# Performance work log

Hardware: AMD Instinct MI355X
Metric: run time of the kernel (lower is better)

Reference implementation:

```python
import jax, jax.numpy as jnp
import numpy as np

EPS = 1e-12  # torch F.normalize default eps


def conv1x1(x, w, b):
    # x: [N,C,H,W], w: [K,C], b: [K]
    return jnp.einsum('nchw,kc->nkhw', x, w) + b[None, :, None, None]


def forward_sa(f1, f2, cw1, cb1, cw2, cb2):
    n, _, h, w = f1.shape
    c1 = conv1x1(f1, cw1, cb1)  # [N,1,H,W]
    c2 = conv1x1(f2, cw2, cb2)
    c1 = jax.nn.softmax(c1.reshape(n, h * w), axis=1).reshape(n, 1, h, w)
    c2 = jax.nn.softmax(c2.reshape(n, h * w), axis=1).reshape(n, 1, h, w)
    return c1 * f1, c2 * f2


def l2norm_ch(x):
    # torch F.normalize(x) -> p=2 over dim=1 with eps clamp
    n = jnp.sqrt(jnp.sum(x * x, axis=1, keepdims=True))
    return x / jnp.maximum(n, EPS)


def forward_ca(f1, f2, pw1, pb1, pw2, pb2):
    N, C, H, W = f1.shape
    f1_cl = conv1x1(f1, pw1, pb1).reshape(N, -1, H * W)  # [N,Cl,HW]
    f2_cl = conv1x1(f2, pw2, pb2).reshape(N, -1, H * W)
    # A[n,p,q] = sum_c f2_cl[n,c,p] * f1_cl[n,c,q]  -> [N,HW,HW]
    A_c = jnp.tanh(jnp.einsum('ncp,ncq->npq', f2_cl, f1_cl))
    f1_v = f1.reshape(N, C, H * W)
    f2_v = f2.reshape(N, C, H * W)
    # f1_hat = f1_v @ A_c^T ; f2_hat = f2_v @ A_c
    f1_hat = jnp.einsum('ncp,nqp->ncq', f1_v, A_c).reshape(N, C, H, W)
    f2_hat = jnp.einsum('ncp,npq->ncq', f2_v, A_c).reshape(N, C, H, W)
    return l2norm_ch(f1_hat), l2norm_ch(f2_hat)


def setup_inputs() -> dict:
    key = jax.random.key(0)
    ks = jax.random.split(key, 10)
    N, C, H, W = 2, 256, 64, 64
    Cl = C // 16
    sc = 1.0 / np.sqrt(C)
    return {
        'f1': jax.random.normal(ks[0], (N, C, H, W), jnp.float32),
        'f2': jax.random.normal(ks[1], (N, C, H, W), jnp.float32),
        'pw1': jax.random.normal(ks[2], (Cl, C), jnp.float32) * sc,
        'pb1': jax.random.normal(ks[3], (Cl,), jnp.float32) * sc,
        'pw2': jax.random.normal(ks[4], (Cl, C), jnp.float32) * sc,
        'pb2': jax.random.normal(ks[5], (Cl,), jnp.float32) * sc,
        'cw1': jax.random.normal(ks[6], (1, C), jnp.float32) * sc,
        'cb1': jax.random.normal(ks[7], (1,), jnp.float32) * sc,
        'cw2': jax.random.normal(ks[8], (1, C), jnp.float32) * sc,
        'cb2': jax.random.normal(ks[9], (1,), jnp.float32) * sc,
    }


def reference(f1, f2, pw1, pb1, pw2, pb2, cw1, cb1, cw2, cb2):
    f1_1, f2_1 = forward_sa(f1, f2, cw1, cb1, cw2, cb2)
    f1_hat, f2_hat = forward_ca(f1_1, f2_1, pw1, pb1, pw2, pb2)
    fp1_hat = jax.nn.relu(f1_hat + f1)
    fp2_hat = jax.nn.relu(f2_hat + f2)
    f1_2, f2_2 = forward_sa(fp1_hat, fp2_hat, cw1, cb1, cw2, cb2)
    # Original calls forward_ca(f1_2, f2_2) again but discards the result
    # and returns (f1_2, f2_2); the dead call is omitted (identical output).
    return (f1_2, f2_2)
```

## Files before the change

### kernel.cpp

```cpp
#include <hip/hip_runtime.h>
#include <hip/hip_bf16.h>
#include <math.h>

#define N_B 2
#define C_CH 256
#define HW_SZ 4096
#define CL_CH 16

typedef __bf16 bf16x8 __attribute__((ext_vector_type(8)));
typedef float f32x4 __attribute__((ext_vector_type(4)));
typedef float f32x16 __attribute__((ext_vector_type(16)));

__device__ __forceinline__ unsigned short f2bf(float x){
  __hip_bfloat16 b = __float2bfloat16(x);
  return *reinterpret_cast<unsigned short*>(&b);
}
__device__ __forceinline__ unsigned int pack_bf2(float a, float b){
  return (unsigned int)f2bf(a) | ((unsigned int)f2bf(b) << 16);
}
__device__ __forceinline__ float tanh_fast(float x){
  float e = __expf(2.0f * x);
  return 1.0f - 2.0f / (1.0f + e);
}
__device__ __forceinline__ void gload16(const void* gsrc, void* lds_dst){
  __builtin_amdgcn_global_load_lds(
      (const __attribute__((address_space(1))) unsigned int*)gsrc,
      (__attribute__((address_space(3))) unsigned int*)lds_dst, 16, 0, 0);
}

__global__ void k_conv1(const float* __restrict__ f1, const float* __restrict__ f2,
                        const float* __restrict__ w1, const float* __restrict__ w2,
                        const float* __restrict__ b1, const float* __restrict__ b2,
                        float* __restrict__ cv){
  const int i = blockIdx.z, n = blockIdx.y, t = threadIdx.x;
  const int ql = t & 63, cg = t >> 6;
  const int q = blockIdx.x * 64 + ql;
  const float* f = (i ? f2 : f1) + n * C_CH * HW_SZ;
  const float* w = i ? w2 : w1;
  __shared__ float ws[C_CH];
  __shared__ float red[4][72];
  ws[t] = w[t];
  __syncthreads();
  float acc = 0.f;
  #pragma unroll 8
  for (int c = cg * 64; c < cg * 64 + 64; ++c)
    acc += f[c * HW_SZ + q] * ws[c];
  red[cg][ql] = acc;
  __syncthreads();
  if (t < 64){
    float s = red[0][t] + red[1][t] + red[2][t] + red[3][t] + (i ? b2[0] : b1[0]);
    cv[(i * 2 + n) * HW_SZ + blockIdx.x * 64 + t] = s;
  }
}

__global__ void k_softmax(const float* __restrict__ cv, float* __restrict__ pr){
  const int r = blockIdx.x, t = threadIdx.x;
  const float* x = cv + r * HW_SZ;
  float* y = pr + r * HW_SZ;
  __shared__ float red[256];
  float v[16];
  float m = -1e30f;
  #pragma unroll
  for (int j = 0; j < 16; j++){ v[j] = x[j * 256 + t]; m = fmaxf(m, v[j]); }
  red[t] = m; __syncthreads();
  for (int s = 128; s > 0; s >>= 1){ if (t < s) red[t] = fmaxf(red[t], red[t + s]); __syncthreads(); }
  m = red[0]; __syncthreads();
  float sum = 0.f;
  #pragma unroll
  for (int j = 0; j < 16; j++){ v[j] = __expf(v[j] - m); sum += v[j]; }
  red[t] = sum; __syncthreads();
  for (int s = 128; s > 0; s >>= 1){ if (t < s) red[t] += red[t + s]; __syncthreads(); }
  const float inv = 1.0f / red[0];
  #pragma unroll
  for (int j = 0; j < 16; j++) y[j * 256 + t] = v[j] * inv;
}

__global__ void k_scale_cl(const float* __restrict__ f1, const float* __restrict__ f2,
                           const float* __restrict__ pr,
                           const float* __restrict__ pw1, const float* __restrict__ pw2,
                           const float* __restrict__ pb1, const float* __restrict__ pb2,
                           unsigned short* __restrict__ fs1, unsigned short* __restrict__ fs2,
                           unsigned short* __restrict__ clT1, unsigned short* __restrict__ clT2){
  const int i = blockIdx.z, n = blockIdx.y, t = threadIdx.x;
  const int ql = t & 63, cg = t >> 6;
  const int q = blockIdx.x * 64 + ql;
  const float* f = (i ? f2 : f1) + n * C_CH * HW_SZ;
  unsigned short* fs = (i ? fs2 : fs1) + n * C_CH * HW_SZ;
  unsigned short* clT = (i ? clT2 : clT1) + n * 32 * HW_SZ;
  const float* pw = i ? pw2 : pw1;
  const float* pb = i ? pb2 : pb1;
  __shared__ float wls[CL_CH * C_CH];
  __shared__ float red[4][CL_CH][66];
  #pragma unroll
  for (int j = 0; j < 16; j++) wls[j * 256 + t] = pw[j * 256 + t];
  __syncthreads();
  const float p = pr[(i * 2 + n) * HW_SZ + q];
  float acc[16];
  #pragma unroll
  for (int k = 0; k < 16; k++) acc[k] = 0.f;
  for (int c = cg * 64; c < cg * 64 + 64; ++c){
    float vv = f[c * HW_SZ + q] * p;
    fs[c * HW_SZ + q] = f2bf(vv);
    #pragma unroll
    for (int k = 0; k < 16; k++) acc[k] += wls[k * 256 + c] * vv;
  }
  #pragma unroll
  for (int k = 0; k < 16; k++) red[cg][k][ql] = acc[k];
  __syncthreads();
  #pragma unroll
  for (int j = 0; j < 4; j++){
    int e = j * 256 + t; int k = e >> 6, qq = e & 63;
    float s = red[0][k][qq] + red[1][k][qq] + red[2][k][qq] + red[3][k][qq] + pb[k];
    clT[(blockIdx.x * 64 + qq) * 32 + k] = f2bf(s);
  }
  if (t < 128){
    uint4 zv = {0u, 0u, 0u, 0u};
    int qq = t >> 1, half = t & 1;
    *reinterpret_cast<uint4*>(&clT[(blockIdx.x * 64 + qq) * 32 + 16 + half * 8]) = zv;
  }
}

__global__ __launch_bounds__(512, 2) void k_hat(
    const unsigned short* __restrict__ fs1, const unsigned short* __restrict__ fs2,
    const unsigned short* __restrict__ clT1, const unsigned short* __restrict__ clT2,
    float* __restrict__ hat1, float* __restrict__ hat2,
    float* __restrict__ pt1, float* __restrict__ pt2){
  const int t = threadIdx.x;
  const int bid = blockIdx.x;
  const int xcd = bid & 7, slot = bid >> 3;
  const int z = xcd >> 1;
  const int n = z & 1, i = z >> 1;
  const int x = slot * 2 + (xcd & 1);
  const int qt = x >> 1, ph = x & 1;
  const int q0 = qt * 128;
  const int pbase = ph * 2048;

  const unsigned short* fs = (i ? fs2 : fs1) + n * C_CH * HW_SZ;
  const unsigned short* uT = (i ? clT1 : clT2) + n * 32 * HW_SZ;
  const unsigned short* vT = (i ? clT2 : clT1) + n * 32 * HW_SZ;
  float* out = (ph ? (i ? pt2 : pt1) : (i ? hat2 : hat1)) + n * C_CH * HW_SZ;

  __shared__ __align__(16) unsigned short fsA[2][C_CH * 64];
  __shared__ __align__(16) unsigned short vB[2][64 * 32];
  __shared__ __align__(16) unsigned short aT[128 * 64];

  const int wv = t >> 6, l = t & 63;
  const int g4 = l >> 4, lr16 = l & 15;
  const int g2 = l >> 5, lr32 = l & 31;

  const int pfw = wv & 3;
  const int qfb = (wv >> 2) * 4;
  const int cblk = wv & 3, qblk = wv >> 2;

  bf16x8 ub0 = *reinterpret_cast<const bf16x8*>(&uT[(q0 + (qfb + 0) * 16 + lr16) * 32 + g4 * 8]);
  bf16x8 ub1 = *reinterpret_cast<const bf16x8*>(&uT[(q0 + (qfb + 1) * 16 + lr16) * 32 + g4 * 8]);
  bf16x8 ub2 = *reinterpret_cast<const bf16x8*>(&uT[(q0 + (qfb + 2) * 16 + lr16) * 32 + g4 * 8]);
  bf16x8 ub3 = *reinterpret_cast<const bf16x8*>(&uT[(q0 + (qfb + 3) * 16 + lr16) * 32 + g4 * 8]);

  f32x16 acc00, acc01, acc10, acc11;
  #pragma unroll
  for (int r = 0; r < 16; ++r){ acc00[r] = 0.f; acc01[r] = 0.f; acc10[r] = 0.f; acc11[r] = 0.f; }
  const f32x4 zz = {0.f, 0.f, 0.f, 0.f};

  int fs_src[4];
  #pragma unroll
  for (int it = 0; it < 4; ++it){
    int d = it * 512 + t; int c = d >> 3, s = d & 7;
    int u = s ^ (c & 7) ^ (((c >> 3) & 1) << 2);
    fs_src[it] = c * (HW_SZ * 2) + u * 16;
  }
  int vt_src;
  {
    int j = t & 255; int p = j >> 2, s = j & 3;
    int u = s ^ (p & 3) ^ ((p >> 2) & 3);
    vt_src = p * 64 + u * 16;
  }
  int vbr;
  {
    int p = pfw * 16 + lr16;
    vbr = p * 64 + ((g4 ^ (p & 3) ^ ((p >> 2) & 3)) << 4);
  }
  unsigned atw0;
  {
    int qd = qfb * 16 + lr16;
    int sw = (pfw * 2 + (g4 >> 1)) ^ (qd & 7) ^ (((qd >> 3) & 1) << 2);
    atw0 = qd * 128 + sw * 16 + (g4 & 1) * 8;
  }
  unsigned afo[2], bqo[2];
  #pragma unroll
  for (int cfi = 0; cfi < 2; ++cfi){
    int crow = cblk * 64 + cfi * 32 + lr32;
    afo[cfi] = crow * 128 + ((g2 ^ (crow & 7) ^ (((crow >> 3) & 1) << 2)) << 4);
  }
  #pragma unroll
  for (int qq = 0; qq < 2; ++qq){
    int qrow = qblk * 64 + qq * 32 + lr32;
    bqo[qq] = qrow * 128 + ((g2 ^ (qrow & 7) ^ (((qrow >> 3) & 1) << 2)) << 4);
  }

  const char* fsb[2] = {(const char*)&fsA[0][0], (const char*)&fsA[1][0]};
  const char* vbb[2] = {(const char*)&vB[0][0], (const char*)&vB[1][0]};
  char* atb = (char*)&aT[0];

  auto stage_fs = [&](unsigned short* dstbase, int p0){
    const char* src = (const char*)fs + p0 * 2;
    #pragma unroll
    for (int it = 0; it < 4; ++it)
      gload16(src + fs_src[it], dstbase + (it * 512 + wv * 64) * 8);
  };
  auto stage_v = [&](unsigned short* dstbase, int p0){
    if (wv < 4)
      gload16((const char*)vT + p0 * 64 + vt_src, dstbase + wv * 512);
  };
  auto dgen = [&](const char* vbB){
    bf16x8 av = *reinterpret_cast<const bf16x8*>(vbB + vbr);
    f32x4 d0 = __builtin_amdgcn_mfma_f32_16x16x32_bf16(av, ub0, zz, 0, 0, 0);
    f32x4 d1 = __builtin_amdgcn_mfma_f32_16x16x32_bf16(av, ub1, zz, 0, 0, 0);
    f32x4 d2 = __builtin_amdgcn_mfma_f32_16x16x32_bf16(av, ub2, zz, 0, 0, 0);
    f32x4 d3 = __builtin_amdgcn_mfma_f32_16x16x32_bf16(av, ub3, zz, 0, 0, 0);
    uint2 pk;
    pk.x = pack_bf2(tanh_fast(d0[0]), tanh_fast(d0[1]));
    pk.y = pack_bf2(tanh_fast(d0[2]), tanh_fast(d0[3]));
    *reinterpret_cast<uint2*>(atb + atw0) = pk;
    pk.x = pack_bf2(tanh_fast(d1[0]), tanh_fast(d1[1]));
    pk.y = pack_bf2(tanh_fast(d1[2]), tanh_fast(d1[3]));
    *reinterpret_cast<uint2*>(atb + atw0 + 2048) = pk;
    pk.x = pack_bf2(tanh_fast(d2[0]), tanh_fast(d2[1]));
    pk.y = pack_bf2(tanh_fast(d2[2]), tanh_fast(d2[3]));
    *reinterpret_cast<uint2*>(atb + atw0 + 4096) = pk;
    pk.x = pack_bf2(tanh_fast(d3[0]), tanh_fast(d3[1]));
    pk.y = pack_bf2(tanh_fast(d3[2]), tanh_fast(d3[3]));
    *reinterpret_cast<uint2*>(atb + atw0 + 6144) = pk;
  };
  auto mmain = [&](const char* faB){
    #pragma unroll
    for (int ks = 0; ks < 4; ++ks){
      unsigned kx = (unsigned)(ks << 5);
      bf16x8 a0 = *reinterpret_cast<const bf16x8*>(faB + (afo[0] ^ kx));
      bf16x8 a1 = *reinterpret_cast<const bf16x8*>(faB + (afo[1] ^ kx));
      bf16x8 b0 = *reinterpret_cast<const bf16x8*>(atb + (bqo[0] ^ kx));
      bf16x8 b1 = *reinterpret_cast<const bf16x8*>(atb + (bqo[1] ^ kx));
      acc00 = __builtin_amdgcn_mfma_f32_32x32x16_bf16(a0, b0, acc00, 0, 0, 0);
      acc01 = __builtin_amdgcn_mfma_f32_32x32x16_bf16(a0, b1, acc01, 0, 0, 0);
      acc10 = __builtin_amdgcn_mfma_f32_32x32x16_bf16(a1, b0, acc10, 0, 0, 0);
      acc11 = __builtin_amdgcn_mfma_f32_32x32x16_bf16(a1, b1, acc11, 0, 0, 0);
    }
  };

  stage_fs(fsA[0], pbase);
  stage_v(vB[0], pbase);
  __syncthreads();

  #pragma unroll 1
  for (int k2 = 0; k2 < 16; ++k2){
    {
      const int p0n = pbase + (2 * k2 + 1) * 64;
      stage_fs(fsA[1], p0n);
      stage_v(vB[1], p0n);
      dgen(vbb[0]);
      asm volatile("s_waitcnt lgkmcnt(0)" ::: "memory");
      __builtin_amdgcn_sched_barrier(0);
      __builtin_amdgcn_s_barrier();
      mmain(fsb[0]);
      __syncthreads();
    }
    {
      const int p0n = pbase + (2 * k2 + 2) * 64;
      stage_fs(fsA[0], p0n);
      stage_v(vB[0], p0n);
      dgen(vbb[1]);
      asm volatile("s_waitcnt lgkmcnt(0)" ::: "memory");
      __builtin_amdgcn_sched_barrier(0);
      __builtin_amdgcn_s_barrier();
      mmain(fsb[1]);
      __syncthreads();
    }
  }

  #pragma unroll
  for (int r = 0; r < 16; ++r){
    int cr = (r & 3) + 8 * (r >> 2) + 4 * g2;
    out[(cblk * 64 + 0 * 32 + cr) * HW_SZ + q0 + qblk * 64 + 0 * 32 + lr32] = acc00[r];
    out[(cblk * 64 + 0 * 32 + cr) * HW_SZ + q0 + qblk * 64 + 1 * 32 + lr32] = acc01[r];
    out[(cblk * 64 + 1 * 32 + cr) * HW_SZ + q0 + qblk * 64 + 0 * 32 + lr32] = acc10[r];
    out[(cblk * 64 + 1 * 32 + cr) * HW_SZ + q0 + qblk * 64 + 1 * 32 + lr32] = acc11[r];
  }
}

__global__ void k_norm(float* __restrict__ hat1, float* __restrict__ hat2,
                       const float* __restrict__ pt1, const float* __restrict__ pt2,
                       const float* __restrict__ f1, const float* __restrict__ f2,
                       const float* __restrict__ cw1, const float* __restrict__ cw2,
                       const float* __restrict__ cb1, const float* __restrict__ cb2,
                       float* __restrict__ cv2){
  const int i = blockIdx.z, n = blockIdx.y, t = threadIdx.x;
  const int ql = t & 63, cg = t >> 6;
  const int q = blockIdx.x * 64 + ql;
  float* hat = (i ? hat2 : hat1) + n * C_CH * HW_SZ;
  const float* pt = (i ? pt2 : pt1) + n * C_CH * HW_SZ;
  const float* f = (i ? f2 : f1) + n * C_CH * HW_SZ;
  __shared__ float ws[C_CH];
  __shared__ float red[4][72];
  __shared__ float invs[64];
  ws[t] = (i ? cw2 : cw1)[t];
  __syncthreads();
  float s = 0.f;
  #pragma unroll 8
  for (int c = cg * 64; c < cg * 64 + 64; ++c){
    float h = hat[c * HW_SZ + q] + pt[c * HW_SZ + q];
    s += h * h;
  }
  red[cg][ql] = s; __syncthreads();
  if (t < 64){
    float ss = red[0][t] + red[1][t] + red[2][t] + red[3][t];
    invs[t] = 1.0f / fmaxf(sqrtf(ss), 1e-12f);
  }
  __syncthreads();
  const float inv = invs[ql];
  float ca = 0.f;
  #pragma unroll 8
  for (int c = cg * 64; c < cg * 64 + 64; ++c){
    float h = hat[c * HW_SZ + q] + pt[c * HW_SZ + q];
    float vv = fmaxf(h * inv + f[c * HW_SZ + q], 0.0f);
    hat[c * HW_SZ + q] = vv;
    ca += ws[c] * vv;
  }
  red[cg][ql] = ca; __syncthreads();
  if (t < 64){
    float ss = red[0][t] + red[1][t] + red[2][t] + red[3][t] + (i ? cb2[0] : cb1[0]);
    cv2[(i * 2 + n) * HW_SZ + blockIdx.x * 64 + t] = ss;
  }
}

__global__ void k_final(const float* __restrict__ fp1, const float* __restrict__ fp2,
                        const float* __restrict__ pr2, float* __restrict__ outp){
  const int i = blockIdx.z;
  const int idx4 = (blockIdx.x * 256 + threadIdx.x) * 4;
  const int n = idx4 >> 20;
  const int q = idx4 & (HW_SZ - 1);
  const float* fp = i ? fp2 : fp1;
  float4 vv = *reinterpret_cast<const float4*>(&fp[idx4]);
  float4 pp = *reinterpret_cast<const float4*>(&pr2[(i * 2 + n) * HW_SZ + q]);
  float4 o; o.x = vv.x * pp.x; o.y = vv.y * pp.y; o.z = vv.z * pp.z; o.w = vv.w * pp.w;
  *reinterpret_cast<float4*>(&outp[i * (C_CH * HW_SZ * N_B) + idx4]) = o;
}

extern "C" void kernel_launch(void* const* d_in, const int* in_sizes, int n_in,
                              void* d_out, int out_size, void* d_ws, size_t ws_size,
                              hipStream_t stream){
  const float* f1  = (const float*)d_in[0];
  const float* f2  = (const float*)d_in[1];
  const float* pw1 = (const float*)d_in[2];
  const float* pb1 = (const float*)d_in[3];
  const float* pw2 = (const float*)d_in[4];
  const float* pb2 = (const float*)d_in[5];
  const float* cw1 = (const float*)d_in[6];
  const float* cb1 = (const float*)d_in[7];
  const float* cw2 = (const float*)d_in[8];
  const float* cb2 = (const float*)d_in[9];
  float* ws = (float*)d_ws;
  float* HAT1 = ws;
  float* HAT2 = ws + 2097152;
  float* PT1  = ws + 4194304;
  float* PT2  = ws + 6291456;
  unsigned short* FS1 = (unsigned short*)(ws + 8388608);
  unsigned short* FS2 = (unsigned short*)(ws + 9437184);
  unsigned short* CLT1 = (unsigned short*)(ws + 10485760);
  unsigned short* CLT2 = (unsigned short*)(ws + 10616832);
  float* CV1  = ws + 10747904;
  float* PR1  = ws + 10764288;
  float* CV2  = ws + 10780672;
  float* PR2  = ws + 10797056;
  float* outp = (float*)d_out;

  k_conv1   <<<dim3(64, 2, 2), 256, 0, stream>>>(f1, f2, cw1, cw2, cb1, cb2, CV1);
  k_softmax <<<4, 256, 0, stream>>>(CV1, PR1);
  k_scale_cl<<<dim3(64, 2, 2), 256, 0, stream>>>(f1, f2, PR1, pw1, pw2, pb1, pb2,
                                                 FS1, FS2, CLT1, CLT2);
  k_hat     <<<256, 512, 0, stream>>>(FS1, FS2, CLT1, CLT2, HAT1, HAT2, PT1, PT2);
  k_norm    <<<dim3(64, 2, 2), 256, 0, stream>>>(HAT1, HAT2, PT1, PT2, f1, f2,
                                                 cw1, cw2, cb1, cb2, CV2);
  k_softmax <<<4, 256, 0, stream>>>(CV2, PR2);
  k_final   <<<dim3(2048, 1, 2), 256, 0, stream>>>(HAT1, HAT2, PR2, outp);
}
```

Baseline: 118.6 us.

## Halve k_hat q-tile to 64, double grid, use packed bf16 convert and rcp

Halves the q tile per block in k_hat from 128 to 64 and doubles the grid to 512 blocks, so each wave keeps two accumulators instead of four. Occupancy is raised to 4 blocks per CU through launch bounds, with the aT LDS buffer halved. The tanh uses a hardware reciprocal, and the bf16 packing uses a single v_cvt_pk_bf16_f32 instruction. The goal is more parallelism and latency hiding, at the cost of less reuse: each block restages the full fs and v tiles for only half as many q columns, which doubles that global and LDS traffic.

```diff
diff --git a/kernel.cpp b/kernel.cpp
--- a/kernel.cpp
+++ b/kernel.cpp
@@ -15,12 +15,14 @@
   __hip_bfloat16 b = __float2bfloat16(x);
   return *reinterpret_cast<unsigned short*>(&b);
 }
-__device__ __forceinline__ unsigned int pack_bf2(float a, float b){
-  return (unsigned int)f2bf(a) | ((unsigned int)f2bf(b) << 16);
+__device__ __forceinline__ unsigned int cvtpk(float a, float b){
+  unsigned int r;
+  asm("v_cvt_pk_bf16_f32 %0, %1, %2" : "=v"(r) : "v"(a), "v"(b));
+  return r;
 }
 __device__ __forceinline__ float tanh_fast(float x){
   float e = __expf(2.0f * x);
-  return 1.0f - 2.0f / (1.0f + e);
+  return fmaf(-2.0f, __builtin_amdgcn_rcpf(1.0f + e), 1.0f);
 }
 __device__ __forceinline__ void gload16(const void* gsrc, void* lds_dst){
   __builtin_amdgcn_global_load_lds(
@@ -120,7 +122,7 @@
   }
 }
 
-__global__ __launch_bounds__(512, 2) void k_hat(
+__global__ __launch_bounds__(512, 4) void k_hat(
     const unsigned short* __restrict__ fs1, const unsigned short* __restrict__ fs2,
     const unsigned short* __restrict__ clT1, const unsigned short* __restrict__ clT2,
     float* __restrict__ hat1, float* __restrict__ hat2,
@@ -132,7 +134,7 @@
   const int n = z & 1, i = z >> 1;
   const int x = slot * 2 + (xcd & 1);
   const int qt = x >> 1, ph = x & 1;
-  const int q0 = qt * 128;
+  const int q0 = qt * 64;
   const int pbase = ph * 2048;
 
   const unsigned short* fs = (i ? fs2 : fs1) + n * C_CH * HW_SZ;
@@ -142,24 +144,22 @@
 
   __shared__ __align__(16) unsigned short fsA[2][C_CH * 64];
   __shared__ __align__(16) unsigned short vB[2][64 * 32];
-  __shared__ __align__(16) unsigned short aT[128 * 64];
+  __shared__ __align__(16) unsigned short aT[64 * 64];
 
   const int wv = t >> 6, l = t & 63;
   const int g4 = l >> 4, lr16 = l & 15;
   const int g2 = l >> 5, lr32 = l & 31;
 
   const int pfw = wv & 3;
-  const int qfb = (wv >> 2) * 4;
+  const int qf0 = (wv >> 2) * 2;
   const int cblk = wv & 3, qblk = wv >> 2;
 
-  bf16x8 ub0 = *reinterpret_cast<const bf16x8*>(&uT[(q0 + (qfb + 0) * 16 + lr16) * 32 + g4 * 8]);
-  bf16x8 ub1 = *reinterpret_cast<const bf16x8*>(&uT[(q0 + (qfb + 1) * 16 + lr16) * 32 + g4 * 8]);
-  bf16x8 ub2 = *reinterpret_cast<const bf16x8*>(&uT[(q0 + (qfb + 2) * 16 + lr16) * 32 + g4 * 8]);
-  bf16x8 ub3 = *reinterpret_cast<const bf16x8*>(&uT[(q0 + (qfb + 3) * 16 + lr16) * 32 + g4 * 8]);
-
-  f32x16 acc00, acc01, acc10, acc11;
-  #pragma unroll
-  for (int r = 0; r < 16; ++r){ acc00[r] = 0.f; acc01[r] = 0.f; acc10[r] = 0.f; acc11[r] = 0.f; }
+  const bf16x8 ub0 = *reinterpret_cast<const bf16x8*>(&uT[(q0 + qf0 * 16 + lr16) * 32 + g4 * 8]);
+  const bf16x8 ub1 = *reinterpret_cast<const bf16x8*>(&uT[(q0 + qf0 * 16 + 16 + lr16) * 32 + g4 * 8]);
+
+  f32x16 acc0, acc1;
+  #pragma unroll
+  for (int r = 0; r < 16; ++r){ acc0[r] = 0.f; acc1[r] = 0.f; }
   const f32x4 zz = {0.f, 0.f, 0.f, 0.f};
 
   int fs_src[4];
@@ -182,20 +182,19 @@
   }
   unsigned atw0;
   {
-    int qd = qfb * 16 + lr16;
+    int qd = qf0 * 16 + lr16;
     int sw = (pfw * 2 + (g4 >> 1)) ^ (qd & 7) ^ (((qd >> 3) & 1) << 2);
     atw0 = qd * 128 + sw * 16 + (g4 & 1) * 8;
   }
-  unsigned afo[2], bqo[2];
+  unsigned afo[2], bqo;
   #pragma unroll
   for (int cfi = 0; cfi < 2; ++cfi){
     int crow = cblk * 64 + cfi * 32 + lr32;
     afo[cfi] = crow * 128 + ((g2 ^ (crow & 7) ^ (((crow >> 3) & 1) << 2)) << 4);
   }
-  #pragma unroll
-  for (int qq = 0; qq < 2; ++qq){
-    int qrow = qblk * 64 + qq * 32 + lr32;
-    bqo[qq] = qrow * 128 + ((g2 ^ (qrow & 7) ^ (((qrow >> 3) & 1) << 2)) << 4);
+  {
+    int qrow = qblk * 32 + lr32;
+    bqo = qrow * 128 + ((g2 ^ (qrow & 7) ^ (((qrow >> 3) & 1) << 2)) << 4);
   }
 
   const char* fsb[2] = {(const char*)&fsA[0][0], (const char*)&fsA[1][0]};
@@ -216,34 +215,23 @@
     bf16x8 av = *reinterpret_cast<const bf16x8*>(vbB + vbr);
     f32x4 d0 = __builtin_amdgcn_mfma_f32_16x16x32_bf16(av, ub0, zz, 0, 0, 0);
     f32x4 d1 = __builtin_amdgcn_mfma_f32_16x16x32_bf16(av, ub1, zz, 0, 0, 0);
-    f32x4 d2 = __builtin_amdgcn_mfma_f32_16x16x32_bf16(av, ub2, zz, 0, 0, 0);
-    f32x4 d3 = __builtin_amdgcn_mfma_f32_16x16x32_bf16(av, ub3, zz, 0, 0, 0);
     uint2 pk;
-    pk.x = pack_bf2(tanh_fast(d0[0]), tanh_fast(d0[1]));
-    pk.y = pack_bf2(tanh_fast(d0[2]), tanh_fast(d0[3]));
+    pk.x = cvtpk(tanh_fast(d0[0]), tanh_fast(d0[1]));
+    pk.y = cvtpk(tanh_fast(d0[2]), tanh_fast(d0[3]));
     *reinterpret_cast<uint2*>(atb + atw0) = pk;
-    pk.x = pack_bf2(tanh_fast(d1[0]), tanh_fast(d1[1]));
-    pk.y = pack_bf2(tanh_fast(d1[2]), tanh_fast(d1[3]));
+    pk.x = cvtpk(tanh_fast(d1[0]), tanh_fast(d1[1]));
+    pk.y = cvtpk(tanh_fast(d1[2]), tanh_fast(d1[3]));
     *reinterpret_cast<uint2*>(atb + atw0 + 2048) = pk;
-    pk.x = pack_bf2(tanh_fast(d2[0]), tanh_fast(d2[1]));
-    pk.y = pack_bf2(tanh_fast(d2[2]), tanh_fast(d2[3]));
-    *reinterpret_cast<uint2*>(atb + atw0 + 4096) = pk;
-    pk.x = pack_bf2(tanh_fast(d3[0]), tanh_fast(d3[1]));
-    pk.y = pack_bf2(tanh_fast(d3[2]), tanh_fast(d3[3]));
-    *reinterpret_cast<uint2*>(atb + atw0 + 6144) = pk;
   };
   auto mmain = [&](const char* faB){
     #pragma unroll
     for (int ks = 0; ks < 4; ++ks){
       unsigned kx = (unsigned)(ks << 5);
+      bf16x8 b0 = *reinterpret_cast<const bf16x8*>(atb + (bqo ^ kx));
       bf16x8 a0 = *reinterpret_cast<const bf16x8*>(faB + (afo[0] ^ kx));
       bf16x8 a1 = *reinterpret_cast<const bf16x8*>(faB + (afo[1] ^ kx));
-      bf16x8 b0 = *reinterpret_cast<const bf16x8*>(atb + (bqo[0] ^ kx));
-      bf16x8 b1 = *reinterpret_cast<const bf16x8*>(atb + (bqo[1] ^ kx));
-      acc00 = __builtin_amdgcn_mfma_f32_32x32x16_bf16(a0, b0, acc00, 0, 0, 0);
-      acc01 = __builtin_amdgcn_mfma_f32_32x32x16_bf16(a0, b1, acc01, 0, 0, 0);
-      acc10 = __builtin_amdgcn_mfma_f32_32x32x16_bf16(a1, b0, acc10, 0, 0, 0);
-      acc11 = __builtin_amdgcn_mfma_f32_32x32x16_bf16(a1, b1, acc11, 0, 0, 0);
+      acc0 = __builtin_amdgcn_mfma_f32_32x32x16_bf16(a0, b0, acc0, 0, 0, 0);
+      acc1 = __builtin_amdgcn_mfma_f32_32x32x16_bf16(a1, b0, acc1, 0, 0, 0);
     }
   };
 
@@ -277,13 +265,12 @@
     }
   }
 
+  const int qcol = q0 + qblk * 32 + lr32;
   #pragma unroll
   for (int r = 0; r < 16; ++r){
     int cr = (r & 3) + 8 * (r >> 2) + 4 * g2;
-    out[(cblk * 64 + 0 * 32 + cr) * HW_SZ + q0 + qblk * 64 + 0 * 32 + lr32] = acc00[r];
-    out[(cblk * 64 + 0 * 32 + cr) * HW_SZ + q0 + qblk * 64 + 1 * 32 + lr32] = acc01[r];
-    out[(cblk * 64 + 1 * 32 + cr) * HW_SZ + q0 + qblk * 64 + 0 * 32 + lr32] = acc10[r];
-    out[(cblk * 64 + 1 * 32 + cr) * HW_SZ + q0 + qblk * 64 + 1 * 32 + lr32] = acc11[r];
+    out[(cblk * 64 + cr) * HW_SZ + qcol] = acc0[r];
+    out[(cblk * 64 + 32 + cr) * HW_SZ + qcol] = acc1[r];
   }
 }
 
@@ -377,7 +364,7 @@
   k_softmax <<<4, 256, 0, stream>>>(CV1, PR1);
   k_scale_cl<<<dim3(64, 2, 2), 256, 0, stream>>>(f1, f2, PR1, pw1, pw2, pb1, pb2,
                                                  FS1, FS2, CLT1, CLT2);
-  k_hat     <<<256, 512, 0, stream>>>(FS1, FS2, CLT1, CLT2, HAT1, HAT2, PT1, PT2);
+  k_hat     <<<512, 512, 0, stream>>>(FS1, FS2, CLT1, CLT2, HAT1, HAT2, PT1, PT2);
   k_norm    <<<dim3(64, 2, 2), 256, 0, stream>>>(HAT1, HAT2, PT1, PT2, f1, f2,
                                                  cw1, cw2, cb1, cb2, CV2);
   k_softmax <<<4, 256, 0, stream>>>(CV2, PR2);
```

Result: faster. 103.9 us (-12.4%).
